# Performance work log

Hardware: AMD Instinct MI355X
Metric: run time of the kernel (lower is better)

## Reference

```python
import jax, jax.numpy as jnp
import numpy as np

B, N, D, H, F = 16, 257, 1024, 16, 4096
HD = D // H
EPS = 1e-5
GATING_TEMP = 0.25  # gating_hyperparam for steep_sigmoid
SCALE = HD ** -0.5


def layer_norm(x, g, b):
    mu = jnp.mean(x, axis=-1, keepdims=True)
    var = jnp.mean(jnp.square(x - mu), axis=-1, keepdims=True)
    return (x - mu) * jax.lax.rsqrt(var + EPS) * g + b


def quick_gelu(x):
    return x * jax.nn.sigmoid(1.702 * x)


def setup_inputs() -> dict:
    key = jax.random.key(0)
    ks = jax.random.split(key, 24)
    s = 0.02
    inp = {
        'hidden_states': jax.random.normal(ks[0], (B, N, D), jnp.float32),
        'cached_hidden': jax.random.normal(ks[1], (B, N, D), jnp.float32),
        'cached_q': jax.random.normal(ks[2], (B, N, D), jnp.float32),
        'cached_k': jax.random.normal(ks[3], (B, N, D), jnp.float32),
        'cached_v': jax.random.normal(ks[4], (B, N, D), jnp.float32),
        'ln1_g': jnp.ones((D,), jnp.float32),
        'ln1_b': jnp.zeros((D,), jnp.float32),
        'wq': jax.random.normal(ks[5], (D, D), jnp.float32) * s,
        'bq': jnp.zeros((D,), jnp.float32),
        'wk': jax.random.normal(ks[6], (D, D), jnp.float32) * s,
        'bk': jnp.zeros((D,), jnp.float32),
        'wv': jax.random.normal(ks[7], (D, D), jnp.float32) * s,
        'bv': jnp.zeros((D,), jnp.float32),
        'wo': jax.random.normal(ks[8], (D, D), jnp.float32) * s,
        'bo': jnp.zeros((D,), jnp.float32),
        'ln2_g': jnp.ones((D,), jnp.float32),
        'ln2_b': jnp.zeros((D,), jnp.float32),
        'w1': jax.random.normal(ks[9], (D, F), jnp.float32) * s,
        'b1': jnp.zeros((F,), jnp.float32),
        'w2': jax.random.normal(ks[10], (F, D), jnp.float32) * s,
        'b2': jnp.zeros((D,), jnp.float32),
        'threshold': jnp.float32(0.5),
    }
    return inp


def reference(hidden_states, cached_hidden, cached_q, cached_k, cached_v,
              ln1_g, ln1_b, wq, bq, wk, bk, wv, bv, wo, bo,
              ln2_g, ln2_b, w1, b1, w2, b2, threshold):
    # layer_norm1 + QKV projection (layer_norm1_qkv_projection)
    h_ln = layer_norm(hidden_states, ln1_g, ln1_b)
    q = h_ln @ wq + bq
    k = h_ln @ wk + bk
    v = h_ln @ wv + bv

    # reuse module: cosine^1 similarity vs cached hidden, steep_sigmoid gating
    # against learned threshold; soft gather/scatter blend of cached states.
    num = jnp.sum(cached_hidden * hidden_states, axis=-1)           # [B,N]
    den = (jnp.linalg.norm(cached_hidden, axis=-1)
           * jnp.linalg.norm(hidden_states, axis=-1) + 1e-8)
    sim = num / den                                                 # [B,N]
    gate = jax.nn.sigmoid((sim - threshold) / GATING_TEMP)[..., None]  # [B,N,1]

    hidden = gate * cached_hidden + (1.0 - gate) * hidden_states
    q = gate * cached_q + (1.0 - gate) * q
    k = gate * cached_k + (1.0 - gate) * k
    v = gate * cached_v + (1.0 - gate) * v

    # manual bmm-softmax-bmm attention
    qh = (q * SCALE).reshape(B, N, H, HD).transpose(0, 2, 1, 3)  # [B,H,N,hd]
    kh = k.reshape(B, N, H, HD).transpose(0, 2, 1, 3)
    vh = v.reshape(B, N, H, HD).transpose(0, 2, 1, 3)
    scores = jnp.einsum('bhqd,bhkd->bhqk', qh, kh)
    probs = jax.nn.softmax(scores, axis=-1)
    attn = jnp.einsum('bhqk,bhkd->bhqd', probs, vh)
    attn = attn.transpose(0, 2, 1, 3).reshape(B, N, D)
    attn = attn @ wo + bo

    hidden = hidden + attn
    residual = hidden
    hidden = layer_norm(hidden, ln2_g, ln2_b)
    hidden = quick_gelu(hidden @ w1 + b1) @ w2 + b2
    return residual + hidden
```

## Files before the change

### kernel.cpp

```cpp
#include <hip/hip_runtime.h>
#include <hip/hip_bf16.h>
#include <stdint.h>

#define BB   16
#define SEQ  257
#define DD   1024
#define NH   16
#define HD_  64
#define FF   4096
#define MM   (BB*SEQ)
#define MPAD 4224
#define SPAD 272
#define VPAD 288
#define SCALE_Q 0.125f

typedef __bf16 bf16x8 __attribute__((ext_vector_type(8)));
typedef float  f32x4  __attribute__((ext_vector_type(4)));
typedef unsigned short u16;

__device__ __forceinline__ u16 f2bf(float f) {
  uint32_t u = __float_as_uint(f);
  uint32_t r = (u + 0x7FFFu + ((u >> 16) & 1u)) >> 16;
  return (u16)r;
}
__device__ __forceinline__ void gll16(const void* g, void* l) {
  __builtin_amdgcn_global_load_lds(
      (const __attribute__((address_space(1))) void*)g,
      (__attribute__((address_space(3))) void*)l, 16, 0, 0);
}
__device__ __forceinline__ float wsum(float v) {
  #pragma unroll
  for (int o = 1; o < 64; o <<= 1) v += __shfl_xor(v, o);
  return v;
}

__global__ __launch_bounds__(256) void transpose_kernel(
    const float* __restrict__ in, u16* __restrict__ out, int R, int C) {
  __shared__ float tile[64][65];
  int ctiles = C >> 6;
  int r0 = (blockIdx.x / ctiles) << 6, c0 = (blockIdx.x % ctiles) << 6;
  int tx = threadIdx.x & 63, ty = threadIdx.x >> 6;
  #pragma unroll
  for (int it = 0; it < 16; ++it) {
    int rr = it * 4 + ty;
    tile[rr][tx] = in[(size_t)(r0 + rr) * C + c0 + tx];
  }
  __syncthreads();
  #pragma unroll
  for (int it = 0; it < 16; ++it) {
    int rr = it * 4 + ty;
    out[(size_t)(c0 + rr) * R + r0 + tx] = f2bf(tile[tx][rr]);
  }
}

__global__ __launch_bounds__(256) void vtrans_kernel(
    const u16* __restrict__ vb, u16* __restrict__ vt) {
  __shared__ u16 tile[64][72];
  const int bh = blockIdx.x, c = blockIdx.y;
  const int tx = threadIdx.x & 63, ty = threadIdx.x >> 6;
  const u16* src = vb + (size_t)bh * SPAD * HD_;
  u16* dst = vt + (size_t)bh * HD_ * VPAD;
  #pragma unroll
  for (int it = 0; it < 16; ++it) {
    int r = it * 4 + ty;
    int nn = c * 64 + r;  int nnc = nn < SPAD ? nn : SPAD - 1;
    tile[r][tx] = src[(size_t)nnc * HD_ + tx];
  }
  __syncthreads();
  #pragma unroll
  for (int it = 0; it < 16; ++it) {
    int hd = it * 4 + ty;
    int col = c * 64 + tx;
    if (col < VPAD) dst[(size_t)hd * VPAD + col] = tile[tx][hd];
  }
}

__global__ __launch_bounds__(256) void ln1_gate_kernel(
    const float* __restrict__ h, const float* __restrict__ c,
    const float* __restrict__ g, const float* __restrict__ bta,
    const float* __restrict__ thr, u16* __restrict__ hln,
    float* __restrict__ hblend, float* __restrict__ gate) {
  int m = blockIdx.x, t = threadIdx.x, l = t & 63, w = t >> 6;
  const float4 hv = *(const float4*)(h + (size_t)m * DD + t * 4);
  const float4 cv = *(const float4*)(c + (size_t)m * DD + t * 4);
  float sh = hv.x + hv.y + hv.z + hv.w;
  float sh2 = hv.x*hv.x + hv.y*hv.y + hv.z*hv.z + hv.w*hv.w;
  float sch = hv.x*cv.x + hv.y*cv.y + hv.z*cv.z + hv.w*cv.w;
  float sc2 = cv.x*cv.x + cv.y*cv.y + cv.z*cv.z + cv.w*cv.w;
  sh = wsum(sh); sh2 = wsum(sh2); sch = wsum(sch); sc2 = wsum(sc2);
  __shared__ float red[4][4];
  if (l == 0) { red[w][0]=sh; red[w][1]=sh2; red[w][2]=sch; red[w][3]=sc2; }
  __syncthreads();
  float Sh  = red[0][0]+red[1][0]+red[2][0]+red[3][0];
  float Sh2 = red[0][1]+red[1][1]+red[2][1]+red[3][1];
  float Sch = red[0][2]+red[1][2]+red[2][2]+red[3][2];
  float Sc2 = red[0][3]+red[1][3]+red[2][3]+red[3][3];
  float mean = Sh * (1.f/DD);
  float var  = Sh2 * (1.f/DD) - mean*mean;
  float rs   = rsqrtf(var + 1e-5f);
  float sim  = Sch / (sqrtf(Sc2)*sqrtf(Sh2) + 1e-8f);
  float gv   = 1.f / (1.f + __expf(-(sim - thr[0]) * 4.0f));
  float4 gg = *(const float4*)(g + t*4);
  float4 bb = *(const float4*)(bta + t*4);
  ushort4 ob;
  ob.x = f2bf((hv.x-mean)*rs*gg.x + bb.x);
  ob.y = f2bf((hv.y-mean)*rs*gg.y + bb.y);
  ob.z = f2bf((hv.z-mean)*rs*gg.z + bb.z);
  ob.w = f2bf((hv.w-mean)*rs*gg.w + bb.w);
  *(ushort4*)(hln + (size_t)m * DD + t * 4) = ob;
  float4 hb;
  hb.x = gv*cv.x + (1.f-gv)*hv.x;  hb.y = gv*cv.y + (1.f-gv)*hv.y;
  hb.z = gv*cv.z + (1.f-gv)*hv.z;  hb.w = gv*cv.w + (1.f-gv)*hv.w;
  *(float4*)(hblend + (size_t)m * DD + t * 4) = hb;
  if (t == 0) gate[m] = gv;
}

__global__ __launch_bounds__(256) void ln2_kernel(
    const float* __restrict__ in, const float* __restrict__ g,
    const float* __restrict__ bta, u16* __restrict__ outb) {
  int m = blockIdx.x, t = threadIdx.x, l = t & 63, w = t >> 6;
  const float4 hv = *(const float4*)(in + (size_t)m * DD + t * 4);
  float sh = hv.x + hv.y + hv.z + hv.w;
  float sh2 = hv.x*hv.x + hv.y*hv.y + hv.z*hv.z + hv.w*hv.w;
  sh = wsum(sh); sh2 = wsum(sh2);
  __shared__ float red[4][2];
  if (l == 0) { red[w][0] = sh; red[w][1] = sh2; }
  __syncthreads();
  float Sh  = red[0][0]+red[1][0]+red[2][0]+red[3][0];
  float Sh2 = red[0][1]+red[1][1]+red[2][1]+red[3][1];
  float mean = Sh * (1.f/DD);
  float rs = rsqrtf(Sh2 * (1.f/DD) - mean*mean + 1e-5f);
  float4 gg = *(const float4*)(g + t*4);
  float4 bb = *(const float4*)(bta + t*4);
  ushort4 ob;
  ob.x = f2bf((hv.x-mean)*rs*gg.x + bb.x);
  ob.y = f2bf((hv.y-mean)*rs*gg.y + bb.y);
  ob.z = f2bf((hv.z-mean)*rs*gg.z + bb.z);
  ob.w = f2bf((hv.w-mean)*rs*gg.w + bb.w);
  *(ushort4*)(outb + (size_t)m * DD + t * 4) = ob;
}

template<int EPI>
__global__ __launch_bounds__(256) void gemm_bt(
    const u16* __restrict__ A, const u16* __restrict__ Bt, int K,
    const float* __restrict__ bias,
    const float* __restrict__ gate,
    const float* __restrict__ c0, const float* __restrict__ c1, const float* __restrict__ c2,
    const float* __restrict__ bq, const float* __restrict__ bk, const float* __restrict__ bv,
    u16* __restrict__ qb, u16* __restrict__ kb, u16* __restrict__ vb,
    const float* __restrict__ addsrc, float* __restrict__ outf, u16* __restrict__ outb) {
  const int tid = threadIdx.x, w = tid >> 6, l = tid & 63, lr = l & 15, lh = l >> 4;
  const int n0 = blockIdx.x * 128, m0 = blockIdx.y * 128;
  const int wm = w >> 1, wn = w & 1;
  __shared__ u16 sA[2][4096], sB[2][4096];
  f32x4 acc[4][4];
  f32x4 zero = {0.f, 0.f, 0.f, 0.f};
  #pragma unroll
  for (int i = 0; i < 4; ++i)
    #pragma unroll
    for (int j = 0; j < 4; ++j) acc[i][j] = zero;

  const int r0 = tid >> 2, cc = (tid & 3) * 8;
  const u16* ga0 = A  + (size_t)(m0 + r0) * K + cc;
  const u16* ga1 = A  + (size_t)(m0 + 64 + r0) * K + cc;
  const u16* gb0 = Bt + (size_t)(n0 + r0) * K + cc;
  const u16* gb1 = Bt + (size_t)(n0 + 64 + r0) * K + cc;

  const int nt = K >> 5;
  gll16(ga0, &sA[0][w*512]);  gll16(ga1, &sA[0][2048 + w*512]);
  gll16(gb0, &sB[0][w*512]);  gll16(gb1, &sB[0][2048 + w*512]);

  for (int t = 0; t < nt; ++t) {
    const int cur = t & 1;
    __syncthreads();
    if (t + 1 < nt) {
      const int k0 = (t + 1) << 5;
      gll16(ga0 + k0, &sA[cur^1][w*512]);  gll16(ga1 + k0, &sA[cur^1][2048 + w*512]);
      gll16(gb0 + k0, &sB[cur^1][w*512]);  gll16(gb1 + k0, &sB[cur^1][2048 + w*512]);
    }
    bf16x8 af[4], bfr[4];
    #pragma unroll
    for (int mi = 0; mi < 4; ++mi)
      af[mi] = *(const bf16x8*)&sA[cur][(wm*64 + mi*16 + lr)*32 + lh*8];
    #pragma unroll
    for (int ni = 0; ni < 4; ++ni)
      bfr[ni] = *(const bf16x8*)&sB[cur][(wn*64 + ni*16 + lr)*32 + lh*8];
    #pragma unroll
    for (int mi = 0; mi < 4; ++mi)
      #pragma unroll
      for (int ni = 0; ni < 4; ++ni)
        acc[mi][ni] = __builtin_amdgcn_mfma_f32_16x16x32_bf16(af[mi], bfr[ni], acc[mi][ni], 0, 0, 0);
  }

  if constexpr (EPI == 0) {
    const int which = n0 >> 10;
    const float* cb = which==0 ? bq : (which==1 ? bk : bv);
    const float* cp = which==0 ? c0 : (which==1 ? c1 : c2);
    u16* dst = which==0 ? qb : (which==1 ? kb : vb);
    const float scl = which==0 ? SCALE_Q : 1.0f;
    #pragma unroll
    for (int mi = 0; mi < 4; ++mi) {
      #pragma unroll
      for (int r = 0; r < 4; ++r) {
        const int row = m0 + wm*64 + mi*16 + lh*4 + r;
        if (row < MM) {
          const float gv = gate[row];
          const int bidx = row / SEQ, nn = row - bidx * SEQ;
          #pragma unroll
          for (int ni = 0; ni < 4; ++ni) {
            const int col = n0 + wn*64 + ni*16 + lr;
            const int d = col & 1023, hd = d & 63, hh = d >> 6;
            const float lin = acc[mi][ni][r] + cb[d];
            const float val = (gv * cp[(size_t)row*DD + d] + (1.f - gv) * lin) * scl;
            dst[((size_t)(bidx*NH + hh)*SPAD + nn)*HD_ + hd] = f2bf(val);
          }
        }
      }
    }
  } else if constexpr (EPI == 1) {
    #pragma unroll
    for (int mi = 0; mi < 4; ++mi)
      #pragma unroll
      for (int r = 0; r < 4; ++r) {
        const int row = m0 + wm*64 + mi*16 + lh*4 + r;
        if (row < MM) {
          #pragma unroll
          for (int ni = 0; ni < 4; ++ni) {
            const int col = n0 + wn*64 + ni*16 + lr;
            outf[(size_t)row*DD + col] = acc[mi][ni][r] + bias[col] + addsrc[(size_t)row*DD + col];
          }
        }
      }
  } else {
    #pragma unroll
    for (int mi = 0; mi < 4; ++mi)
      #pragma unroll
      for (int r = 0; r < 4; ++r) {
        const int row = m0 + wm*64 + mi*16 + lh*4 + r;
        if (row < MM) {
          #pragma unroll
          for (int ni = 0; ni < 4; ++ni) {
            const int col = n0 + wn*64 + ni*16 + lr;
            const float x = acc[mi][ni][r] + bias[col];
            const float s = 1.f / (1.f + __expf(-1.702f * x));
            outb[(size_t)row*FF + col] = f2bf(x * s);
          }
        }
      }
  }
}

__global__ __launch_bounds__(256) void attn_kernel(
    const u16* __restrict__ qb, const u16* __restrict__ kb,
    const u16* __restrict__ vt, u16* __restrict__ attn_out) {
  __shared__ u16 P[64 * 296];
  const int bh = blockIdx.x, b = bh >> 4, hh = bh & 15;
  const int q0 = blockIdx.y * 64;
  const int tid = threadIdx.x, w = tid >> 6, l = tid & 63, lr = l & 15, lh = l >> 4;
  const u16* qp = qb + (size_t)bh * SPAD * HD_;
  const u16* kp = kb + (size_t)bh * SPAD * HD_;
  const u16* vp = vt + (size_t)bh * HD_ * VPAD;

  const int qr = q0 + w*16 + lr;
  const int qrc = qr < 271 ? qr : 271;
  bf16x8 aq0 = *(const bf16x8*)(qp + (size_t)qrc*HD_ + lh*8);
  bf16x8 aq1 = *(const bf16x8*)(qp + (size_t)qrc*HD_ + 32 + lh*8);

  f32x4 st[18];
  f32x4 zero = {0.f,0.f,0.f,0.f};
  #pragma unroll
  for (int t = 0; t < 18; ++t) st[t] = zero;
  #pragma unroll
  for (int t = 0; t < 18; ++t) {
    int key = t*16 + lr;  int keyc = key < 271 ? key : 271;
    bf16x8 b0 = *(const bf16x8*)(kp + (size_t)keyc*HD_ + lh*8);
    bf16x8 b1 = *(const bf16x8*)(kp + (size_t)keyc*HD_ + 32 + lh*8);
    st[t] = __builtin_amdgcn_mfma_f32_16x16x32_bf16(aq0, b0, st[t], 0, 0, 0);
    st[t] = __builtin_amdgcn_mfma_f32_16x16x32_bf16(aq1, b1, st[t], 0, 0, 0);
  }
  #pragma unroll
  for (int t = 0; t < 18; ++t) {
    int key = t*16 + lr;
    if (key >= SEQ) { st[t][0]=-1e30f; st[t][1]=-1e30f; st[t][2]=-1e30f; st[t][3]=-1e30f; }
  }
  float mr[4], sr[4];
  #pragma unroll
  for (int r = 0; r < 4; ++r) {
    float m = st[0][r];
    #pragma unroll
    for (int t = 1; t < 18; ++t) m = fmaxf(m, st[t][r]);
    m = fmaxf(m, __shfl_xor(m, 1));  m = fmaxf(m, __shfl_xor(m, 2));
    m = fmaxf(m, __shfl_xor(m, 4));  m = fmaxf(m, __shfl_xor(m, 8));
    mr[r] = m;  sr[r] = 0.f;
  }
  #pragma unroll
  for (int t = 0; t < 18; ++t)
    #pragma unroll
    for (int r = 0; r < 4; ++r) {
      float p = __expf(st[t][r] - mr[r]);
      st[t][r] = p;  sr[r] += p;
    }
  #pragma unroll
  for (int r = 0; r < 4; ++r) {
    sr[r] += __shfl_xor(sr[r], 1);  sr[r] += __shfl_xor(sr[r], 2);
    sr[r] += __shfl_xor(sr[r], 4);  sr[r] += __shfl_xor(sr[r], 8);
  }
  #pragma unroll
  for (int t = 0; t < 18; ++t)
    #pragma unroll
    for (int r = 0; r < 4; ++r)
      P[(w*16 + lh*4 + r)*296 + t*16 + lr] = f2bf(st[t][r]);
  __syncthreads();

  f32x4 o[4];
  #pragma unroll
  for (int ni = 0; ni < 4; ++ni) o[ni] = zero;
  #pragma unroll
  for (int ks = 0; ks < 9; ++ks) {
    bf16x8 pa = *(const bf16x8*)&P[(w*16 + lr)*296 + ks*32 + lh*8];
    #pragma unroll
    for (int ni = 0; ni < 4; ++ni) {
      bf16x8 bv_ = *(const bf16x8*)(vp + (size_t)(ni*16 + lr)*VPAD + ks*32 + lh*8);
      o[ni] = __builtin_amdgcn_mfma_f32_16x16x32_bf16(pa, bv_, o[ni], 0, 0, 0);
    }
  }
  #pragma unroll
  for (int r = 0; r < 4; ++r) {
    const int qrow = q0 + w*16 + lh*4 + r;
    if (qrow < SEQ) {
      const float inv = 1.f / sr[r];
      #pragma unroll
      for (int ni = 0; ni < 4; ++ni)
        attn_out[(size_t)(b*SEQ + qrow)*DD + hh*HD_ + ni*16 + lr] = f2bf(o[ni][r] * inv);
    }
  }
}

extern "C" void kernel_launch(void* const* d_in, const int* in_sizes, int n_in,
                              void* d_out, int out_size, void* d_ws, size_t ws_size,
                              hipStream_t stream) {
  (void)in_sizes; (void)n_in; (void)out_size; (void)ws_size;
  const float* hidden   = (const float*)d_in[0];
  const float* cached_h = (const float*)d_in[1];
  const float* cached_q = (const float*)d_in[2];
  const float* cached_k = (const float*)d_in[3];
  const float* cached_v = (const float*)d_in[4];
  const float* ln1_g = (const float*)d_in[5];
  const float* ln1_b = (const float*)d_in[6];
  const float* wq = (const float*)d_in[7];
  const float* bq = (const float*)d_in[8];
  const float* wk = (const float*)d_in[9];
  const float* bk = (const float*)d_in[10];
  const float* wv = (const float*)d_in[11];
  const float* bv = (const float*)d_in[12];
  const float* wo = (const float*)d_in[13];
  const float* bo = (const float*)d_in[14];
  const float* ln2_g = (const float*)d_in[15];
  const float* ln2_b = (const float*)d_in[16];
  const float* w1 = (const float*)d_in[17];
  const float* b1 = (const float*)d_in[18];
  const float* w2 = (const float*)d_in[19];
  const float* b2 = (const float*)d_in[20];
  const float* thr = (const float*)d_in[21];
  float* out = (float*)d_out;

  char* ws = (char*)d_ws;
  size_t off = 0;
  auto alloc = [&](size_t bytes) {
    void* p = ws + off;  off += (bytes + 255) & ~(size_t)255;  return p;
  };
  u16*   wqkvT  = (u16*)alloc(3072ull * 1024 * 2);
  u16*   woT    = (u16*)alloc(1024ull * 1024 * 2);
  u16*   w1T    = (u16*)alloc(4096ull * 1024 * 2);
  u16*   w2T    = (u16*)alloc(1024ull * 4096 * 2);
  float* gate   = (float*)alloc((size_t)MPAD * 4);
  float* resid2 = (float*)alloc((size_t)MPAD * DD * 4);
  u16*   regA   = (u16*)alloc((size_t)MPAD * DD * 2);
  u16 *hln = regA, *attn_o = regA, *ln2out = regA;
  const size_t QKV_B = (size_t)256 * SPAD * HD_ * 2;
  const size_t VT_B  = (size_t)256 * HD_ * VPAD * 2;
  char*  regB   = (char*)alloc(3*QKV_B + VT_B + (size_t)MPAD * DD * 4);
  u16*   qbuf   = (u16*)regB;
  u16*   kbuf   = (u16*)(regB + QKV_B);
  u16*   vbuf   = (u16*)(regB + 2*QKV_B);
  u16*   vtb    = (u16*)(regB + 3*QKV_B);
  float* hblend = (float*)(regB + 3*QKV_B + VT_B);
  u16*   mid    = (u16*)regB;

  dim3 blk(256);
  transpose_kernel<<<dim3(256),  blk, 0, stream>>>(wq, wqkvT,                 1024, 1024);
  transpose_kernel<<<dim3(256),  blk, 0, stream>>>(wk, wqkvT + 1024*1024,     1024, 1024);
  transpose_kernel<<<dim3(256),  blk, 0, stream>>>(wv, wqkvT + 2*1024*1024,   1024, 1024);
  transpose_kernel<<<dim3(256),  blk, 0, stream>>>(wo, woT,                   1024, 1024);
  transpose_kernel<<<dim3(1024), blk, 0, stream>>>(w1, w1T,                   1024, 4096);
  transpose_kernel<<<dim3(1024), blk, 0, stream>>>(w2, w2T,                   4096, 1024);

  ln1_gate_kernel<<<dim3(MM), blk, 0, stream>>>(hidden, cached_h, ln1_g, ln1_b, thr,
                                                hln, hblend, gate);

  gemm_bt<0><<<dim3(24, 33), blk, 0, stream>>>(hln, wqkvT, 1024, nullptr,
      gate, cached_q, cached_k, cached_v, bq, bk, bv, qbuf, kbuf, vbuf,
      nullptr, nullptr, nullptr);

  vtrans_kernel<<<dim3(256, 5), blk, 0, stream>>>(vbuf, vtb);

  attn_kernel<<<dim3(256, 5), blk, 0, stream>>>(qbuf, kbuf, vtb, attn_o);

  gemm_bt<1><<<dim3(8, 33), blk, 0, stream>>>(attn_o, woT, 1024, bo,
      nullptr, nullptr, nullptr, nullptr, nullptr, nullptr, nullptr,
      nullptr, nullptr, nullptr, hblend, resid2, nullptr);

  ln2_kernel<<<dim3(MM), blk, 0, stream>>>(resid2, ln2_g, ln2_b, ln2out);

  gemm_bt<2><<<dim3(32, 33), blk, 0, stream>>>(ln2out, w1T, 1024, b1,
      nullptr, nullptr, nullptr, nullptr, nullptr, nullptr, nullptr,
      nullptr, nullptr, nullptr, nullptr, nullptr, mid);

  gemm_bt<1><<<dim3(8, 33), blk, 0, stream>>>(mid, w2T, 4096, b2,
      nullptr, nullptr, nullptr, nullptr, nullptr, nullptr, nullptr,
      nullptr, nullptr, nullptr, resid2, out, nullptr);
}
```

Measured before the change: 332.7 us.

## Fuse weight transposes, swizzle GEMM tile order, split-K the MLP down-projection

Merges the six weight-transpose launches into one kernel. Remaps GEMM workgroup IDs through an XCD-style swizzle with M as the fast grid dimension, to improve L2 locality across chiplets. Splits the K=4096 down-projection GEMM into two halves that write bf16 partial sums, followed by a reduction kernel that adds bias and residual. This raises parallelism for the 264-tile GEMM, but adds an extra pass over memory and extra bf16 rounding of the partial sums.

```diff
diff --git a/kernel.cpp b/kernel.cpp
--- a/kernel.cpp
+++ b/kernel.cpp
@@ -9,7 +9,7 @@
 #define HD_  64
 #define FF   4096
 #define MM   (BB*SEQ)
-#define MPAD 4224
+#define MPAD2 4352
 #define SPAD 272
 #define VPAD 288
 #define SCALE_Q 0.125f
@@ -23,6 +23,9 @@
   uint32_t r = (u + 0x7FFFu + ((u >> 16) & 1u)) >> 16;
   return (u16)r;
 }
+__device__ __forceinline__ float bf2f(u16 u) {
+  return __uint_as_float(((uint32_t)u) << 16);
+}
 __device__ __forceinline__ void gll16(const void* g, void* l) {
   __builtin_amdgcn_global_load_lds(
       (const __attribute__((address_space(1))) void*)g,
@@ -34,22 +37,34 @@
   return v;
 }
 
-__global__ __launch_bounds__(256) void transpose_kernel(
-    const float* __restrict__ in, u16* __restrict__ out, int R, int C) {
+__global__ __launch_bounds__(256) void transpose_all(
+    const float* __restrict__ wq, const float* __restrict__ wk,
+    const float* __restrict__ wv, const float* __restrict__ wo,
+    const float* __restrict__ w1, const float* __restrict__ w2,
+    u16* __restrict__ wqkvT, u16* __restrict__ woT,
+    u16* __restrict__ w1T, u16* __restrict__ w2T) {
   __shared__ float tile[64][65];
-  int ctiles = C >> 6;
-  int r0 = (blockIdx.x / ctiles) << 6, c0 = (blockIdx.x % ctiles) << 6;
-  int tx = threadIdx.x & 63, ty = threadIdx.x >> 6;
+  const int bid = blockIdx.x;
+  const float* src;  u16* dst;  int R, C, b;
+  if (bid < 768)       { int s = bid >> 8;  b = bid & 255;
+                         src = s==0?wq:(s==1?wk:wv);  dst = wqkvT + s*1024*1024;
+                         R = 1024; C = 1024; }
+  else if (bid < 1024) { src = wo;  dst = woT;  b = bid - 768;   R = 1024; C = 1024; }
+  else if (bid < 2048) { src = w1;  dst = w1T;  b = bid - 1024;  R = 1024; C = 4096; }
+  else                 { src = w2;  dst = w2T;  b = bid - 2048;  R = 4096; C = 1024; }
+  const int ctiles = C >> 6;
+  const int r0 = (b / ctiles) << 6, c0 = (b % ctiles) << 6;
+  const int tx = threadIdx.x & 63, ty = threadIdx.x >> 6;
   #pragma unroll
   for (int it = 0; it < 16; ++it) {
     int rr = it * 4 + ty;
-    tile[rr][tx] = in[(size_t)(r0 + rr) * C + c0 + tx];
+    tile[rr][tx] = src[(size_t)(r0 + rr) * C + c0 + tx];
   }
   __syncthreads();
   #pragma unroll
   for (int it = 0; it < 16; ++it) {
     int rr = it * 4 + ty;
-    out[(size_t)(c0 + rr) * R + r0 + tx] = f2bf(tile[tx][rr]);
+    dst[(size_t)(c0 + rr) * R + r0 + tx] = f2bf(tile[tx][rr]);
   }
 }
 
@@ -142,15 +157,22 @@
 
 template<int EPI>
 __global__ __launch_bounds__(256) void gemm_bt(
-    const u16* __restrict__ A, const u16* __restrict__ Bt, int K,
+    const u16* __restrict__ A, const u16* __restrict__ Bt,
+    int Kstride, int Kiter,
     const float* __restrict__ bias,
     const float* __restrict__ gate,
     const float* __restrict__ c0, const float* __restrict__ c1, const float* __restrict__ c2,
     const float* __restrict__ bq, const float* __restrict__ bk, const float* __restrict__ bv,
     u16* __restrict__ qb, u16* __restrict__ kb, u16* __restrict__ vb,
-    const float* __restrict__ addsrc, float* __restrict__ outf, u16* __restrict__ outb) {
+    const float* __restrict__ addsrc, float* __restrict__ outf,
+    u16* __restrict__ outb, u16* __restrict__ partb) {
   const int tid = threadIdx.x, w = tid >> 6, l = tid & 63, lr = l & 15, lh = l >> 4;
-  const int n0 = blockIdx.x * 128, m0 = blockIdx.y * 128;
+  const int Mt = gridDim.x;
+  const int f = blockIdx.y * Mt + blockIdx.x;
+  const int nwg = Mt * gridDim.y;
+  const int swz = (f & 7) * (nwg >> 3) + (f >> 3);
+  const int m0 = (swz % Mt) * 128, n0 = (swz / Mt) * 128;
+  const int kBase = blockIdx.z * Kiter;
   const int wm = w >> 1, wn = w & 1;
   __shared__ u16 sA[2][4096], sB[2][4096];
   f32x4 acc[4][4];
@@ -161,12 +183,12 @@
     for (int j = 0; j < 4; ++j) acc[i][j] = zero;
 
   const int r0 = tid >> 2, cc = (tid & 3) * 8;
-  const u16* ga0 = A  + (size_t)(m0 + r0) * K + cc;
-  const u16* ga1 = A  + (size_t)(m0 + 64 + r0) * K + cc;
-  const u16* gb0 = Bt + (size_t)(n0 + r0) * K + cc;
-  const u16* gb1 = Bt + (size_t)(n0 + 64 + r0) * K + cc;
-
-  const int nt = K >> 5;
+  const u16* ga0 = A  + (size_t)(m0 + r0) * Kstride + kBase + cc;
+  const u16* ga1 = A  + (size_t)(m0 + 64 + r0) * Kstride + kBase + cc;
+  const u16* gb0 = Bt + (size_t)(n0 + r0) * Kstride + kBase + cc;
+  const u16* gb1 = Bt + (size_t)(n0 + 64 + r0) * Kstride + kBase + cc;
+
+  const int nt = Kiter >> 5;
   gll16(ga0, &sA[0][w*512]);  gll16(ga1, &sA[0][2048 + w*512]);
   gll16(gb0, &sB[0][w*512]);  gll16(gb1, &sB[0][2048 + w*512]);
 
@@ -231,7 +253,7 @@
           }
         }
       }
-  } else {
+  } else if constexpr (EPI == 2) {
     #pragma unroll
     for (int mi = 0; mi < 4; ++mi)
       #pragma unroll
@@ -247,7 +269,40 @@
           }
         }
       }
-  }
+  } else {
+    u16* pp = partb + (size_t)blockIdx.z * ((size_t)MPAD2 * 1024);
+    #pragma unroll
+    for (int mi = 0; mi < 4; ++mi)
+      #pragma unroll
+      for (int r = 0; r < 4; ++r) {
+        const int row = m0 + wm*64 + mi*16 + lh*4 + r;
+        if (row < MM) {
+          #pragma unroll
+          for (int ni = 0; ni < 4; ++ni) {
+            const int col = n0 + wn*64 + ni*16 + lr;
+            pp[(size_t)row*1024 + col] = f2bf(acc[mi][ni][r]);
+          }
+        }
+      }
+  }
+}
+
+__global__ __launch_bounds__(256) void reduce_mlp2(
+    const u16* __restrict__ parts, const float* __restrict__ bias,
+    const float* __restrict__ resid, float* __restrict__ out) {
+  const size_t PS = (size_t)MPAD2 * 1024;
+  const int row = blockIdx.x, t = threadIdx.x, c = t * 4;
+  const size_t base = (size_t)row * 1024 + c;
+  float4 r = *(const float4*)(resid + base);
+  float4 b = *(const float4*)(bias + c);
+  float o0 = r.x + b.x, o1 = r.y + b.y, o2 = r.z + b.z, o3 = r.w + b.w;
+  #pragma unroll
+  for (int p = 0; p < 2; ++p) {
+    ushort4 u = *(const ushort4*)(parts + p*PS + base);
+    o0 += bf2f(u.x);  o1 += bf2f(u.y);  o2 += bf2f(u.z);  o3 += bf2f(u.w);
+  }
+  float4 o;  o.x = o0;  o.y = o1;  o.z = o2;  o.w = o3;
+  *(float4*)(out + base) = o;
 }
 
 __global__ __launch_bounds__(256) void attn_kernel(
@@ -373,50 +428,50 @@
   u16*   woT    = (u16*)alloc(1024ull * 1024 * 2);
   u16*   w1T    = (u16*)alloc(4096ull * 1024 * 2);
   u16*   w2T    = (u16*)alloc(1024ull * 4096 * 2);
-  float* gate   = (float*)alloc((size_t)MPAD * 4);
-  float* resid2 = (float*)alloc((size_t)MPAD * DD * 4);
-  u16*   regA   = (u16*)alloc((size_t)MPAD * DD * 2);
+  float* gate   = (float*)alloc((size_t)MPAD2 * 4);
+  float* resid2 = (float*)alloc((size_t)MPAD2 * DD * 4);
+  u16*   regA   = (u16*)alloc((size_t)MPAD2 * DD * 2);
   u16 *hln = regA, *attn_o = regA, *ln2out = regA;
-  const size_t QKV_B = (size_t)256 * SPAD * HD_ * 2;
-  const size_t VT_B  = (size_t)256 * HD_ * VPAD * 2;
-  char*  regB   = (char*)alloc(3*QKV_B + VT_B + (size_t)MPAD * DD * 4);
+  const size_t QKV_B  = (size_t)256 * SPAD * HD_ * 2;
+  const size_t VT_B   = (size_t)256 * HD_ * VPAD * 2;
+  const size_t PART_B = (size_t)MPAD2 * 1024 * 2;
+  const size_t partsOff = 3*QKV_B + VT_B;
+  char*  regB   = (char*)alloc(partsOff + 2*PART_B);
   u16*   qbuf   = (u16*)regB;
   u16*   kbuf   = (u16*)(regB + QKV_B);
   u16*   vbuf   = (u16*)(regB + 2*QKV_B);
   u16*   vtb    = (u16*)(regB + 3*QKV_B);
-  float* hblend = (float*)(regB + 3*QKV_B + VT_B);
+  float* hblend = (float*)(regB + partsOff);
   u16*   mid    = (u16*)regB;
+  u16*   parts  = (u16*)(regB + partsOff);
 
   dim3 blk(256);
-  transpose_kernel<<<dim3(256),  blk, 0, stream>>>(wq, wqkvT,                 1024, 1024);
-  transpose_kernel<<<dim3(256),  blk, 0, stream>>>(wk, wqkvT + 1024*1024,     1024, 1024);
-  transpose_kernel<<<dim3(256),  blk, 0, stream>>>(wv, wqkvT + 2*1024*1024,   1024, 1024);
-  transpose_kernel<<<dim3(256),  blk, 0, stream>>>(wo, woT,                   1024, 1024);
-  transpose_kernel<<<dim3(1024), blk, 0, stream>>>(w1, w1T,                   1024, 4096);
-  transpose_kernel<<<dim3(1024), blk, 0, stream>>>(w2, w2T,                   4096, 1024);
+  transpose_all<<<dim3(3072), blk, 0, stream>>>(wq, wk, wv, wo, w1, w2,
+                                                wqkvT, woT, w1T, w2T);
 
   ln1_gate_kernel<<<dim3(MM), blk, 0, stream>>>(hidden, cached_h, ln1_g, ln1_b, thr,
                                                 hln, hblend, gate);
 
-  gemm_bt<0><<<dim3(24, 33), blk, 0, stream>>>(hln, wqkvT, 1024, nullptr,
+  gemm_bt<0><<<dim3(33, 24), blk, 0, stream>>>(hln, wqkvT, 1024, 1024, nullptr,
       gate, cached_q, cached_k, cached_v, bq, bk, bv, qbuf, kbuf, vbuf,
-      nullptr, nullptr, nullptr);
+      nullptr, nullptr, nullptr, nullptr);
 
   vtrans_kernel<<<dim3(256, 5), blk, 0, stream>>>(vbuf, vtb);
-
   attn_kernel<<<dim3(256, 5), blk, 0, stream>>>(qbuf, kbuf, vtb, attn_o);
 
-  gemm_bt<1><<<dim3(8, 33), blk, 0, stream>>>(attn_o, woT, 1024, bo,
+  gemm_bt<1><<<dim3(33, 8), blk, 0, stream>>>(attn_o, woT, 1024, 1024, bo,
       nullptr, nullptr, nullptr, nullptr, nullptr, nullptr, nullptr,
-      nullptr, nullptr, nullptr, hblend, resid2, nullptr);
+      nullptr, nullptr, nullptr, hblend, resid2, nullptr, nullptr);
 
   ln2_kernel<<<dim3(MM), blk, 0, stream>>>(resid2, ln2_g, ln2_b, ln2out);
 
-  gemm_bt<2><<<dim3(32, 33), blk, 0, stream>>>(ln2out, w1T, 1024, b1,
+  gemm_bt<2><<<dim3(33, 32), blk, 0, stream>>>(ln2out, w1T, 1024, 1024, b1,
       nullptr, nullptr, nullptr, nullptr, nullptr, nullptr, nullptr,
-      nullptr, nullptr, nullptr, nullptr, nullptr, mid);
-
-  gemm_bt<1><<<dim3(8, 33), blk, 0, stream>>>(mid, w2T, 4096, b2,
+      nullptr, nullptr, nullptr, nullptr, nullptr, mid, nullptr);
+
+  gemm_bt<3><<<dim3(33, 8, 2), blk, 0, stream>>>(mid, w2T, 4096, 2048, nullptr,
       nullptr, nullptr, nullptr, nullptr, nullptr, nullptr, nullptr,
-      nullptr, nullptr, nullptr, resid2, out, nullptr);
-}
+      nullptr, nullptr, nullptr, nullptr, nullptr, nullptr, parts);
+
+  reduce_mlp2<<<dim3(MM), blk, 0, stream>>>(parts, b2, resid2, out);
+}
```

After: 313.5 us. 5.8% less time.
